# Performance work log

Measured on AMD Instinct MI355X. Metric: run time of the kernel, lower is better.

## Reference

```python
import jax, jax.numpy as jnp
import numpy as np

DIM = 1024
HEADS = 16
DIM_HEAD = 64
INNER = HEADS * DIM_HEAD  # 1024
SCALE = DIM ** (-0.5)     # NOTE: source uses dim, not dim_head, for scaling


def setup_inputs() -> dict:
    key = jax.random.key(0)
    k_x, k_qkv, k_out = jax.random.split(key, 3)
    x = jax.random.normal(k_x, (4, 2048, DIM), dtype=jnp.float32)
    # store weights pre-transposed: y = x @ W  (equivalent to torch Linear with W.T)
    w_qkv = jax.random.normal(k_qkv, (DIM, 3 * INNER), dtype=jnp.float32) * 0.02
    w_out = jax.random.normal(k_out, (INNER, DIM), dtype=jnp.float32) * 0.02
    b_out = jnp.zeros((DIM,), dtype=jnp.float32)
    return {"x": x, "w_qkv": w_qkv, "w_out": w_out, "b_out": b_out}


def reference(x, w_qkv, w_out, b_out):
    b, n, _ = x.shape
    qkv = x @ w_qkv                                  # [b, n, 3*inner]
    q, k, v = jnp.split(qkv, 3, axis=-1)             # each [b, n, inner]

    def to_heads(t):
        return t.reshape(b, n, HEADS, DIM_HEAD).transpose(0, 2, 1, 3)  # [b, h, n, d]

    q, k, v = to_heads(q), to_heads(k), to_heads(v)
    dots = jnp.einsum("bhid,bhjd->bhij", q, k) * SCALE   # [b, h, n, n]
    attn = jax.nn.softmax(dots, axis=-1)
    out = jnp.einsum("bhij,bhjd->bhid", attn, v)         # [b, h, n, d]
    out = out.transpose(0, 2, 1, 3).reshape(b, n, INNER)  # [b, n, inner]
    return out @ w_out + b_out                            # dropout p=0 -> identity
```

## Files before the change

### kernel.cpp

```cpp
#include <hip/hip_runtime.h>
#include <math.h>

#define BATCH   4
#define NSEQ    2048
#define DIM     1024
#define HEADS   16
#define DHEAD   64
#define INNER   1024
#define MTOT    (BATCH*NSEQ)
#define SC_L2E  0.04508422f

typedef __attribute__((ext_vector_type(8))) unsigned short u16x8;
typedef __attribute__((ext_vector_type(4))) unsigned short u16x4;
typedef __attribute__((ext_vector_type(8))) short          bf16x8;
typedef __attribute__((ext_vector_type(4))) float          f32x4;

__device__ __forceinline__ unsigned short f2bf(float f) {
    unsigned int u = __builtin_bit_cast(unsigned int, f);
    u += 0x7FFFu + ((u >> 16) & 1u);
    return (unsigned short)(u >> 16);
}

__device__ __forceinline__ float fexp2(float x) {
    float r; asm("v_exp_f32 %0, %1" : "=v"(r) : "v"(x)); return r;
}

__device__ __forceinline__ unsigned int cvtpk(float lo, float hi) {
    unsigned int r; asm("v_cvt_pk_bf16_f32 %0, %1, %2" : "=v"(r) : "v"(lo), "v"(hi));
    return r;
}

#define GLDS16(gp, lp) __builtin_amdgcn_global_load_lds( \
    (const __attribute__((address_space(1))) unsigned int*)(gp), \
    (__attribute__((address_space(3))) unsigned int*)(lp), 16, 0, 0)

#define SWC(r, c) ((c) ^ (((r) & 7) << 3))

__global__ __launch_bounds__(256) void prep_fused(const float* __restrict__ x,
                                                  const float* __restrict__ w_qkv,
                                                  const float* __restrict__ w_out,
                                                  unsigned short* __restrict__ Xb,
                                                  unsigned short* __restrict__ Wqt,
                                                  unsigned short* __restrict__ Wot)
{
    __shared__ float tile[32][33];
    const int bid = blockIdx.x;
    if (bid < 4096) {
        const int i = bid * 256 + threadIdx.x;
        const float4* p = reinterpret_cast<const float4*>(x) + (size_t)i * 2;
        float4 a = p[0], b = p[1];
        u16x8 o;
        o[0]=f2bf(a.x); o[1]=f2bf(a.y); o[2]=f2bf(a.z); o[3]=f2bf(a.w);
        o[4]=f2bf(b.x); o[5]=f2bf(b.y); o[6]=f2bf(b.z); o[7]=f2bf(b.w);
        reinterpret_cast<u16x8*>(Xb)[i] = o;
        return;
    }
    const float* in; unsigned short* out; int R, C, bx, by;
    if (bid < 4096 + 3072) {
        const int lin = bid - 4096;
        in = w_qkv; out = Wqt; R = DIM; C = 3 * INNER;
        bx = lin % 96; by = lin / 96;
    } else {
        const int lin = bid - (4096 + 3072);
        in = w_out; out = Wot; R = INNER; C = DIM;
        bx = lin & 31; by = lin >> 5;
    }
    const int c0 = bx * 32, r0 = by * 32;
    const int tx = threadIdx.x & 31, ty = threadIdx.x >> 5;
#pragma unroll
    for (int i = 0; i < 32; i += 8)
        tile[ty + i][tx] = in[(size_t)(r0 + ty + i) * C + c0 + tx];
    __syncthreads();
#pragma unroll
    for (int i = 0; i < 32; i += 8)
        out[(size_t)(c0 + ty + i) * R + r0 + tx] = f2bf(tile[tx][ty + i]);
}

__global__ __launch_bounds__(256) void gemm_qkv_mfma(const unsigned short* __restrict__ A,
                                                     const unsigned short* __restrict__ Bt,
                                                     unsigned short* __restrict__ qb,
                                                     unsigned short* __restrict__ kb,
                                                     unsigned short* __restrict__ vt)
{
    __shared__ unsigned short As[128][64];
    __shared__ unsigned short Bs[128][64];

    const int t = threadIdx.x;
    const int l = t & 63, w = t >> 6;
    const int wr = w >> 1, wc = w & 1;
    const int g = l >> 4, ql = l & 15;

    const int lin  = blockIdx.x + 24 * blockIdx.y;
    const int nlin = (lin & 7) * 192 + (lin >> 3);
    const int bx = nlin % 24, by = nlin / 24;
    const int row0 = by * 128;
    const int col0 = bx * 128;

    const int lr  = l >> 3;
    const int lcg = (l & 7) ^ lr;
    const unsigned short* aBase = A  + (size_t)(row0 + w * 32 + lr) * DIM + lcg * 8;
    const unsigned short* bBase = Bt + (size_t)(col0 + w * 32 + lr) * DIM + lcg * 8;

    f32x4 acc[4][4];
#pragma unroll
    for (int mi = 0; mi < 4; ++mi)
#pragma unroll
        for (int ni = 0; ni < 4; ++ni)
#pragma unroll
            for (int r = 0; r < 4; ++r) acc[mi][ni][r] = 0.f;

    for (int k0 = 0; k0 < DIM; k0 += 64) {
        __syncthreads();
#pragma unroll
        for (int i = 0; i < 4; ++i) {
            GLDS16(aBase + k0 + (size_t)i * 8 * DIM, &As[w * 32 + i * 8][0]);
            GLDS16(bBase + k0 + (size_t)i * 8 * DIM, &Bs[w * 32 + i * 8][0]);
        }
        __syncthreads();

#pragma unroll
        for (int kh = 0; kh < 2; ++kh) {
            bf16x8 af[4], bf[4];
#pragma unroll
            for (int mi = 0; mi < 4; ++mi) {
                const int ar = wr * 64 + mi * 16 + ql;
                af[mi] = *reinterpret_cast<const bf16x8*>(&As[ar][SWC(ar, kh * 32 + g * 8)]);
            }
#pragma unroll
            for (int ni = 0; ni < 4; ++ni) {
                const int br = wc * 64 + ni * 16 + ql;
                bf[ni] = *reinterpret_cast<const bf16x8*>(&Bs[br][SWC(br, kh * 32 + g * 8)]);
            }
#pragma unroll
            for (int mi = 0; mi < 4; ++mi)
#pragma unroll
                for (int ni = 0; ni < 4; ++ni)
                    acc[mi][ni] = __builtin_amdgcn_mfma_f32_16x16x32_bf16(af[mi], bf[ni], acc[mi][ni], 0, 0, 0);
        }
    }

#pragma unroll
    for (int mi = 0; mi < 4; ++mi) {
        const int m0 = row0 + wr * 64 + mi * 16 + g * 4;
        const int b  = m0 >> 11, n0 = m0 & 2047;
#pragma unroll
        for (int ni = 0; ni < 4; ++ni) {
            const int c = col0 + wc * 64 + ni * 16 + ql;
            const int part = c >> 10, inner = c & 1023;
            const int h = inner >> 6, d = inner & 63;
            if (part == 2) {
                const int key0 = n0 & 63;
                const int nst  = (n0 & ~63)
                               | (key0 & 0x23)
                               | (((key0 >> 3) & 1) << 4)
                               | (((key0 >> 2) & 1) << 3)
                               | (((key0 >> 4) & 1) << 2);
                u16x4 pk;
#pragma unroll
                for (int r = 0; r < 4; ++r) pk[r] = f2bf(acc[mi][ni][r]);
                *reinterpret_cast<u16x4*>(&vt[(((size_t)b * HEADS + h) * DHEAD + d) * NSEQ + nst]) = pk;
            } else if (part == 0) {
                unsigned short* dst = qb + (((size_t)b * HEADS + h) * NSEQ + n0) * DHEAD + d;
#pragma unroll
                for (int r = 0; r < 4; ++r) dst[(size_t)r * DHEAD] = f2bf(acc[mi][ni][r] * SC_L2E);
            } else {
                unsigned short* dst = kb + (((size_t)b * HEADS + h) * NSEQ + n0) * DHEAD + d;
#pragma unroll
                for (int r = 0; r < 4; ++r) dst[(size_t)r * DHEAD] = f2bf(acc[mi][ni][r]);
            }
        }
    }
}

__global__ __launch_bounds__(256) void gemm_out_mfma(const unsigned short* __restrict__ A,
                                                     const unsigned short* __restrict__ Bt,
                                                     const float* __restrict__ bias,
                                                     float* __restrict__ out)
{
    __shared__ unsigned short As[128][32];
    __shared__ unsigned short Bs[128][32];

    const int t = threadIdx.x;
    const int l = t & 63, w = t >> 6;
    const int wr = w >> 1, wc = w & 1;
    const int g = l >> 4, ql = l & 15;

    const int lin  = blockIdx.x + 8 * blockIdx.y;
    const int nlin = (lin & 7) * 64 + (lin >> 3);
    const int bx = nlin % 8, by = nlin / 8;
    const int row0 = by * 128;
    const int col0 = bx * 128;
    const int lr  = l >> 2;
    const int lcg = (l & 3) ^ ((l >> 3) & 3);
    const int rsw = (g ^ ((ql >> 1) & 3)) * 8;

    f32x4 acc[4][4];
#pragma unroll
    for (int mi = 0; mi < 4; ++mi)
#pragma unroll
        for (int ni = 0; ni < 4; ++ni)
#pragma unroll
            for (int r = 0; r < 4; ++r) acc[mi][ni][r] = 0.f;

    for (int k0 = 0; k0 < INNER; k0 += 32) {
        __syncthreads();
        {
            const unsigned short* ag = A  + (size_t)(row0 + 32 * w + lr) * INNER + k0 + lcg * 8;
            const unsigned short* bg = Bt + (size_t)(col0 + 32 * w + lr) * INNER + k0 + lcg * 8;
            GLDS16(ag,               &As[32 * w][0]);
            GLDS16(ag + 16 * INNER,  &As[32 * w + 16][0]);
            GLDS16(bg,               &Bs[32 * w][0]);
            GLDS16(bg + 16 * INNER,  &Bs[32 * w + 16][0]);
        }
        __syncthreads();

        bf16x8 af[4], bf[4];
#pragma unroll
        for (int mi = 0; mi < 4; ++mi)
            af[mi] = *reinterpret_cast<const bf16x8*>(&As[wr * 64 + mi * 16 + ql][rsw]);
#pragma unroll
        for (int ni = 0; ni < 4; ++ni)
            bf[ni] = *reinterpret_cast<const bf16x8*>(&Bs[wc * 64 + ni * 16 + ql][rsw]);
#pragma unroll
        for (int mi = 0; mi < 4; ++mi)
#pragma unroll
            for (int ni = 0; ni < 4; ++ni)
                acc[mi][ni] = __builtin_amdgcn_mfma_f32_16x16x32_bf16(af[mi], bf[ni], acc[mi][ni], 0, 0, 0);
    }

#pragma unroll
    for (int mi = 0; mi < 4; ++mi) {
        const int m0 = row0 + wr * 64 + mi * 16 + g * 4;
#pragma unroll
        for (int ni = 0; ni < 4; ++ni) {
            const int c = col0 + wc * 64 + ni * 16 + ql;
            const float bv = bias[c];
#pragma unroll
            for (int r = 0; r < 4; ++r)
                out[(size_t)(m0 + r) * DIM + c] = acc[mi][ni][r] + bv;
        }
    }
}

__global__ __launch_bounds__(512) void attn_mfma(const unsigned short* __restrict__ qg,
                                                 const unsigned short* __restrict__ kg,
                                                 const unsigned short* __restrict__ vtg,
                                                 unsigned short* __restrict__ og)
{
    __shared__ unsigned short Ks [2][64 * 64];
    __shared__ unsigned short Vts[2][64 * 64];

    const int bh = blockIdx.x;
    const int b = bh >> 4, h = bh & 15;
    const int qblk = blockIdx.y;
    const int t = threadIdx.x, l = t & 63, w = t >> 6;
    const int g = l >> 4, ql = l & 15;

    const size_t hb = (size_t)bh * NSEQ * DHEAD;

    bf16x8 qf[2][2];
#pragma unroll
    for (int qh = 0; qh < 2; ++qh) {
        const unsigned short* qrow = qg + hb + (size_t)(qblk * 256 + w * 32 + qh * 16 + ql) * DHEAD;
        qf[qh][0] = *reinterpret_cast<const bf16x8*>(qrow + g * 8);
        qf[qh][1] = *reinterpret_cast<const bf16x8*>(qrow + 32 + g * 8);
    }

    const int srow  = l >> 3;
    const int sslot = (l & 7) ^ srow;
    const unsigned short* kSrc = kg  + hb + (size_t)(w * 8 + srow) * DHEAD + sslot * 8;
    const unsigned short* vSrc = vtg + hb + (size_t)(w * 8 + srow) * NSEQ  + sslot * 8;

    GLDS16(kSrc, &Ks [0][(w * 8) * 64]);
    GLDS16(vSrc, &Vts[0][(w * 8) * 64]);
    __syncthreads();

    f32x4 acc_o[2][4];
#pragma unroll
    for (int qh = 0; qh < 2; ++qh)
#pragma unroll
        for (int dt = 0; dt < 4; ++dt)
#pragma unroll
            for (int rr = 0; rr < 4; ++rr) acc_o[qh][dt][rr] = 0.f;
    float l_r[2] = {0.f, 0.f};

    for (int kbi = 0; kbi < NSEQ / 64; ++kbi) {
        const int cur = kbi & 1;
        if (kbi + 1 < NSEQ / 64) {
            GLDS16(kSrc + (size_t)(kbi + 1) * 64 * DHEAD, &Ks [cur ^ 1][(w * 8) * 64]);
            GLDS16(vSrc + (size_t)(kbi + 1) * 64,         &Vts[cur ^ 1][(w * 8) * 64]);
        }

        f32x4 sacc[2][4];
#pragma unroll
        for (int qh = 0; qh < 2; ++qh)
#pragma unroll
            for (int jt = 0; jt < 4; ++jt)
#pragma unroll
                for (int rr = 0; rr < 4; ++rr) sacc[qh][jt][rr] = 0.f;
        __builtin_amdgcn_s_setprio(1);
#pragma unroll
        for (int jt = 0; jt < 4; ++jt) {
            const int row = jt * 16 + ql;
            bf16x8 kf0 = *reinterpret_cast<const bf16x8*>(&Ks[cur][row * 64 + SWC(row, g * 8)]);
            bf16x8 kf1 = *reinterpret_cast<const bf16x8*>(&Ks[cur][row * 64 + SWC(row, 32 + g * 8)]);
            sacc[0][jt] = __builtin_amdgcn_mfma_f32_16x16x32_bf16(kf0, qf[0][0], sacc[0][jt], 0, 0, 0);
            sacc[0][jt] = __builtin_amdgcn_mfma_f32_16x16x32_bf16(kf1, qf[0][1], sacc[0][jt], 0, 0, 0);
            sacc[1][jt] = __builtin_amdgcn_mfma_f32_16x16x32_bf16(kf0, qf[1][0], sacc[1][jt], 0, 0, 0);
            sacc[1][jt] = __builtin_amdgcn_mfma_f32_16x16x32_bf16(kf1, qf[1][1], sacc[1][jt], 0, 0, 0);
        }
        __builtin_amdgcn_s_setprio(0);

        bf16x8 pf[2][2];
#pragma unroll
        for (int qh = 0; qh < 2; ++qh) {
            float p[16];
#pragma unroll
            for (int jt = 0; jt < 4; ++jt)
#pragma unroll
                for (int rr = 0; rr < 4; ++rr)
                    p[jt * 4 + rr] = fexp2(sacc[qh][jt][rr]);
            float s0 = (p[0] + p[1]) + (p[2] + p[3]);
            float s1 = (p[4] + p[5]) + (p[6] + p[7]);
            float s2 = (p[8] + p[9]) + (p[10] + p[11]);
            float s3 = (p[12] + p[13]) + (p[14] + p[15]);
            l_r[qh] += (s0 + s1) + (s2 + s3);

#pragma unroll
            for (int js = 0; js < 2; ++js) {
                unsigned int u0 = cvtpk(p[8 * js + 0], p[8 * js + 1]);
                unsigned int u1 = cvtpk(p[8 * js + 2], p[8 * js + 3]);
                unsigned int u2 = cvtpk(p[8 * js + 4], p[8 * js + 5]);
                unsigned int u3 = cvtpk(p[8 * js + 6], p[8 * js + 7]);
                uint4 uu = {u0, u1, u2, u3};
                pf[qh][js] = __builtin_bit_cast(bf16x8, uu);
            }
        }

        __builtin_amdgcn_s_setprio(1);
#pragma unroll
        for (int js = 0; js < 2; ++js) {
            bf16x8 vf[4];
#pragma unroll
            for (int dt = 0; dt < 4; ++dt) {
                const int row = dt * 16 + ql;
                vf[dt] = *reinterpret_cast<const bf16x8*>(&Vts[cur][row * 64 + SWC(row, js * 32 + g * 8)]);
            }
#pragma unroll
            for (int qh = 0; qh < 2; ++qh)
#pragma unroll
                for (int dt = 0; dt < 4; ++dt)
                    acc_o[qh][dt] = __builtin_amdgcn_mfma_f32_16x16x32_bf16(vf[dt], pf[qh][js], acc_o[qh][dt], 0, 0, 0);
        }
        __builtin_amdgcn_s_setprio(0);

        __syncthreads();
    }

#pragma unroll
    for (int qh = 0; qh < 2; ++qh) {
        float lt = l_r[qh];
        lt += __shfl_xor(lt, 16);
        lt += __shfl_xor(lt, 32);
        const float rinv = 1.0f / lt;
        const int n = qblk * 256 + w * 32 + qh * 16 + ql;
        unsigned short* dst = og + ((size_t)b * NSEQ + n) * INNER + h * DHEAD;
#pragma unroll
        for (int dt = 0; dt < 4; ++dt) {
            uint2 u;
            u.x = cvtpk(acc_o[qh][dt][0] * rinv, acc_o[qh][dt][1] * rinv);
            u.y = cvtpk(acc_o[qh][dt][2] * rinv, acc_o[qh][dt][3] * rinv);
            *reinterpret_cast<uint2*>(&dst[dt * 16 + g * 4]) = u;
        }
    }
}


extern "C" void kernel_launch(void* const* d_in, const int* in_sizes, int n_in,
                              void* d_out, int out_size, void* d_ws, size_t ws_size,
                              hipStream_t stream) {
    const float* x     = (const float*)d_in[0];
    const float* w_qkv = (const float*)d_in[1];
    const float* w_out = (const float*)d_in[2];
    const float* b_out = (const float*)d_in[3];
    float* out = (float*)d_out;

    unsigned short* ws = (unsigned short*)d_ws;
    const size_t nX  = (size_t)MTOT * DIM;
    const size_t nWq = (size_t)DIM * 3 * INNER;
    const size_t nWo = (size_t)DIM * INNER;
    unsigned short* Xb  = ws;
    unsigned short* Wqt = Xb  + nX;
    unsigned short* Wot = Wqt + nWq;
    unsigned short* qb  = Wot + nWo;
    unsigned short* kb  = qb  + nX;
    unsigned short* vt  = kb  + nX;
    unsigned short* Ob  = vt  + nX;

    prep_fused<<<dim3(4096 + 3072 + 1024), dim3(256), 0, stream>>>(x, w_qkv, w_out, Xb, Wqt, Wot);
    gemm_qkv_mfma<<<dim3(3 * INNER / 128, MTOT / 128), dim3(256), 0, stream>>>(Xb, Wqt, qb, kb, vt);
    attn_mfma<<<dim3(BATCH * HEADS, NSEQ / 256), dim3(512), 0, stream>>>(qb, kb, vt, Ob);
    gemm_out_mfma<<<dim3(DIM / 128, MTOT / 128), dim3(256), 0, stream>>>(Ob, Wot, b_out, out);
}
```

Measured before the change: 174.2 us.

## Deepen attention K/V prefetch to two tiles and widen out-projection K tile

The attention kernel now uses four K/V shared-memory buffers and prefetches two tiles ahead, so it only needs a barrier every other iteration. Score accumulators now start from a zero constant instead of being zeroed explicitly. The output GEMM steps through K in chunks of 64 instead of 32, using a new XOR swizzle and two MFMA sub-steps per tile. This halves its barrier count. The aim is to cut synchronisation overhead and hide more global-load latency, at the cost of doubling LDS use in both kernels, which may lower occupancy.

Result: slower. 180.5 us (+3.6%).

```diff
diff --git a/kernel.cpp b/kernel.cpp
--- a/kernel.cpp
+++ b/kernel.cpp
@@ -177,8 +177,8 @@
                                                      const float* __restrict__ bias,
                                                      float* __restrict__ out)
 {
-    __shared__ unsigned short As[128][32];
-    __shared__ unsigned short Bs[128][32];
+    __shared__ unsigned short As[128][64];
+    __shared__ unsigned short Bs[128][64];
 
     const int t = threadIdx.x;
     const int l = t & 63, w = t >> 6;
@@ -190,9 +190,11 @@
     const int bx = nlin % 8, by = nlin / 8;
     const int row0 = by * 128;
     const int col0 = bx * 128;
-    const int lr  = l >> 2;
-    const int lcg = (l & 3) ^ ((l >> 3) & 3);
-    const int rsw = (g ^ ((ql >> 1) & 3)) * 8;
+
+    const int lr  = l >> 3;
+    const int lcg = (l & 7) ^ lr;
+    const unsigned short* aBase = A  + (size_t)(row0 + w * 32 + lr) * INNER + lcg * 8;
+    const unsigned short* bBase = Bt + (size_t)(col0 + w * 32 + lr) * INNER + lcg * 8;
 
     f32x4 acc[4][4];
 #pragma unroll
@@ -202,30 +204,34 @@
 #pragma unroll
             for (int r = 0; r < 4; ++r) acc[mi][ni][r] = 0.f;
 
-    for (int k0 = 0; k0 < INNER; k0 += 32) {
+    for (int k0 = 0; k0 < INNER; k0 += 64) {
         __syncthreads();
-        {
-            const unsigned short* ag = A  + (size_t)(row0 + 32 * w + lr) * INNER + k0 + lcg * 8;
-            const unsigned short* bg = Bt + (size_t)(col0 + 32 * w + lr) * INNER + k0 + lcg * 8;
-            GLDS16(ag,               &As[32 * w][0]);
-            GLDS16(ag + 16 * INNER,  &As[32 * w + 16][0]);
-            GLDS16(bg,               &Bs[32 * w][0]);
-            GLDS16(bg + 16 * INNER,  &Bs[32 * w + 16][0]);
+#pragma unroll
+        for (int i = 0; i < 4; ++i) {
+            GLDS16(aBase + k0 + (size_t)i * 8 * INNER, &As[w * 32 + i * 8][0]);
+            GLDS16(bBase + k0 + (size_t)i * 8 * INNER, &Bs[w * 32 + i * 8][0]);
         }
         __syncthreads();
 
-        bf16x8 af[4], bf[4];
-#pragma unroll
-        for (int mi = 0; mi < 4; ++mi)
-            af[mi] = *reinterpret_cast<const bf16x8*>(&As[wr * 64 + mi * 16 + ql][rsw]);
-#pragma unroll
-        for (int ni = 0; ni < 4; ++ni)
-            bf[ni] = *reinterpret_cast<const bf16x8*>(&Bs[wc * 64 + ni * 16 + ql][rsw]);
-#pragma unroll
-        for (int mi = 0; mi < 4; ++mi)
-#pragma unroll
-            for (int ni = 0; ni < 4; ++ni)
-                acc[mi][ni] = __builtin_amdgcn_mfma_f32_16x16x32_bf16(af[mi], bf[ni], acc[mi][ni], 0, 0, 0);
+#pragma unroll
+        for (int kh = 0; kh < 2; ++kh) {
+            bf16x8 af[4], bf[4];
+#pragma unroll
+            for (int mi = 0; mi < 4; ++mi) {
+                const int ar = wr * 64 + mi * 16 + ql;
+                af[mi] = *reinterpret_cast<const bf16x8*>(&As[ar][SWC(ar, kh * 32 + g * 8)]);
+            }
+#pragma unroll
+            for (int ni = 0; ni < 4; ++ni) {
+                const int br = wc * 64 + ni * 16 + ql;
+                bf[ni] = *reinterpret_cast<const bf16x8*>(&Bs[br][SWC(br, kh * 32 + g * 8)]);
+            }
+#pragma unroll
+            for (int mi = 0; mi < 4; ++mi)
+#pragma unroll
+                for (int ni = 0; ni < 4; ++ni)
+                    acc[mi][ni] = __builtin_amdgcn_mfma_f32_16x16x32_bf16(af[mi], bf[ni], acc[mi][ni], 0, 0, 0);
+        }
     }
 
 #pragma unroll
@@ -247,8 +253,8 @@
                                                  const unsigned short* __restrict__ vtg,
                                                  unsigned short* __restrict__ og)
 {
-    __shared__ unsigned short Ks [2][64 * 64];
-    __shared__ unsigned short Vts[2][64 * 64];
+    __shared__ unsigned short Ks [4][64 * 64];
+    __shared__ unsigned short Vts[4][64 * 64];
 
     const int bh = blockIdx.x;
     const int b = bh >> 4, h = bh & 15;
@@ -271,9 +277,13 @@
     const unsigned short* kSrc = kg  + hb + (size_t)(w * 8 + srow) * DHEAD + sslot * 8;
     const unsigned short* vSrc = vtg + hb + (size_t)(w * 8 + srow) * NSEQ  + sslot * 8;
 
-    GLDS16(kSrc, &Ks [0][(w * 8) * 64]);
-    GLDS16(vSrc, &Vts[0][(w * 8) * 64]);
+    GLDS16(kSrc,                    &Ks [0][(w * 8) * 64]);
+    GLDS16(vSrc,                    &Vts[0][(w * 8) * 64]);
+    GLDS16(kSrc + 64 * DHEAD,       &Ks [1][(w * 8) * 64]);
+    GLDS16(vSrc + 64,               &Vts[1][(w * 8) * 64]);
     __syncthreads();
+
+    const f32x4 zf = {0.f, 0.f, 0.f, 0.f};
 
     f32x4 acc_o[2][4];
 #pragma unroll
@@ -285,29 +295,23 @@
     float l_r[2] = {0.f, 0.f};
 
     for (int kbi = 0; kbi < NSEQ / 64; ++kbi) {
-        const int cur = kbi & 1;
-        if (kbi + 1 < NSEQ / 64) {
-            GLDS16(kSrc + (size_t)(kbi + 1) * 64 * DHEAD, &Ks [cur ^ 1][(w * 8) * 64]);
-            GLDS16(vSrc + (size_t)(kbi + 1) * 64,         &Vts[cur ^ 1][(w * 8) * 64]);
+        const int buf = kbi & 3;
+        if (kbi + 2 < NSEQ / 64) {
+            GLDS16(kSrc + (size_t)(kbi + 2) * 64 * DHEAD, &Ks [(kbi + 2) & 3][(w * 8) * 64]);
+            GLDS16(vSrc + (size_t)(kbi + 2) * 64,         &Vts[(kbi + 2) & 3][(w * 8) * 64]);
         }
 
         f32x4 sacc[2][4];
-#pragma unroll
-        for (int qh = 0; qh < 2; ++qh)
-#pragma unroll
-            for (int jt = 0; jt < 4; ++jt)
-#pragma unroll
-                for (int rr = 0; rr < 4; ++rr) sacc[qh][jt][rr] = 0.f;
         __builtin_amdgcn_s_setprio(1);
 #pragma unroll
         for (int jt = 0; jt < 4; ++jt) {
             const int row = jt * 16 + ql;
-            bf16x8 kf0 = *reinterpret_cast<const bf16x8*>(&Ks[cur][row * 64 + SWC(row, g * 8)]);
-            bf16x8 kf1 = *reinterpret_cast<const bf16x8*>(&Ks[cur][row * 64 + SWC(row, 32 + g * 8)]);
-            sacc[0][jt] = __builtin_amdgcn_mfma_f32_16x16x32_bf16(kf0, qf[0][0], sacc[0][jt], 0, 0, 0);
-            sacc[0][jt] = __builtin_amdgcn_mfma_f32_16x16x32_bf16(kf1, qf[0][1], sacc[0][jt], 0, 0, 0);
-            sacc[1][jt] = __builtin_amdgcn_mfma_f32_16x16x32_bf16(kf0, qf[1][0], sacc[1][jt], 0, 0, 0);
-            sacc[1][jt] = __builtin_amdgcn_mfma_f32_16x16x32_bf16(kf1, qf[1][1], sacc[1][jt], 0, 0, 0);
+            bf16x8 kf0 = *reinterpret_cast<const bf16x8*>(&Ks[buf][row * 64 + SWC(row, g * 8)]);
+            bf16x8 kf1 = *reinterpret_cast<const bf16x8*>(&Ks[buf][row * 64 + SWC(row, 32 + g * 8)]);
+            f32x4 t0 = __builtin_amdgcn_mfma_f32_16x16x32_bf16(kf0, qf[0][0], zf, 0, 0, 0);
+            sacc[0][jt] = __builtin_amdgcn_mfma_f32_16x16x32_bf16(kf1, qf[0][1], t0, 0, 0, 0);
+            f32x4 t1 = __builtin_amdgcn_mfma_f32_16x16x32_bf16(kf0, qf[1][0], zf, 0, 0, 0);
+            sacc[1][jt] = __builtin_amdgcn_mfma_f32_16x16x32_bf16(kf1, qf[1][1], t1, 0, 0, 0);
         }
         __builtin_amdgcn_s_setprio(0);
 
@@ -344,7 +348,7 @@
 #pragma unroll
             for (int dt = 0; dt < 4; ++dt) {
                 const int row = dt * 16 + ql;
-                vf[dt] = *reinterpret_cast<const bf16x8*>(&Vts[cur][row * 64 + SWC(row, js * 32 + g * 8)]);
+                vf[dt] = *reinterpret_cast<const bf16x8*>(&Vts[buf][row * 64 + SWC(row, js * 32 + g * 8)]);
             }
 #pragma unroll
             for (int qh = 0; qh < 2; ++qh)
@@ -354,7 +358,7 @@
         }
         __builtin_amdgcn_s_setprio(0);
 
-        __syncthreads();
+        if (kbi & 1) __syncthreads();
     }
 
 #pragma unroll
```
